# Optimization experiments

Hardware: AMD Instinct MI355X
Metric: run time of the kernel (lower is better)

## Reference

```python
import jax, jax.numpy as jnp
import numpy as np

# Fixed problem geometry: B equal-sized graphs with contiguous node ids.
B, N, E, F_IN, H, C = 64, 1024, 655360, 128, 128, 10
K1 = int(np.ceil(0.8 * N))    # 820 nodes/graph kept by pool1
K2 = int(np.ceil(0.8 * K1))   # 656 nodes/graph kept by pool2


def setup_inputs() -> dict:
    key = jax.random.key(0)
    ks = jax.random.split(key, 12)
    x = jax.random.normal(ks[0], (B * N, F_IN), jnp.float32)
    # intra-graph random edges, E//B per graph
    e_per = E // B
    local = jax.random.randint(ks[1], (2, E), 0, N)
    off = jnp.repeat(jnp.arange(B, dtype=jnp.int32) * N, e_per)
    edge_index = (local + off[None, :]).astype(jnp.int32)
    batch = jnp.repeat(jnp.arange(B, dtype=jnp.int32), N)

    def lin(k, i, o):
        return jax.random.normal(k, (i, o), jnp.float32) / np.sqrt(i)

    return {
        "x": x, "edge_index": edge_index, "batch": batch,
        "Wl1": lin(ks[2], F_IN, H), "bl1": jnp.zeros((H,), jnp.float32), "Wr1": lin(ks[3], F_IN, H),
        "Wl2": lin(ks[4], H, H),    "bl2": jnp.zeros((H,), jnp.float32), "Wr2": lin(ks[5], H, H),
        "pw1": jax.random.normal(ks[6], (H,), jnp.float32) / np.sqrt(H),
        "pw2": jax.random.normal(ks[7], (H,), jnp.float32) / np.sqrt(H),
        "fW1": lin(ks[8], 2 * H, H), "fb1": jnp.zeros((H,), jnp.float32),
        "fW2": lin(ks[9], H, C),     "fb2": jnp.zeros((C,), jnp.float32),
    }


def _sage(x, src, dst, em, Wl, bl, Wr, n):
    # PyG SAGEConv (aggr='mean'): lin_l(mean_{j->i} x_j) + lin_r(x_i)
    msg = x[src] * em[:, None]                                   # [E, d]
    s = jax.ops.segment_sum(msg, dst, num_segments=n)            # [n, d]
    cnt = jax.ops.segment_sum(em, dst, num_segments=n)           # [n]
    mean = s / jnp.maximum(cnt, 1.0)[:, None]
    return mean @ Wl + bl + x @ Wr


def _topk_pool(x, src, dst, em, n_per, k, w):
    # PyG TopKPooling: score = tanh(x.w/||w||); keep top-k per graph; gate kept x by score.
    score = jnp.tanh(x @ w / jnp.linalg.norm(w))                 # [B*n_per]
    _, idx = jax.lax.top_k(score.reshape(B, n_per), k)           # [B, k]
    idx = jnp.sort(idx, axis=1)
    perm = (idx + (jnp.arange(B) * n_per)[:, None]).reshape(-1)  # global kept ids [B*k]
    nx = x[perm] * score[perm][:, None]
    # relabel edges; drop edges touching removed nodes via mask
    inv = jnp.full((B * n_per,), -1, jnp.int32).at[perm].set(jnp.arange(B * k, dtype=jnp.int32))
    ns, nd = inv[src], inv[dst]
    nm = em * (ns >= 0).astype(x.dtype) * (nd >= 0).astype(x.dtype)
    return nx, jnp.maximum(ns, 0), jnp.maximum(nd, 0), nm


def _readout(h, k):
    g = h.reshape(B, k, H)
    return jnp.concatenate([g.mean(axis=1), g.max(axis=1)], axis=1)  # [B, 2H]


def reference(x, edge_index, batch, Wl1, bl1, Wr1, Wl2, bl2, Wr2,
              pw1, pw2, fW1, fb1, fW2, fb2):
    src, dst = edge_index[0], edge_index[1]
    em = jnp.ones((E,), x.dtype)
    h = jax.nn.relu(_sage(x, src, dst, em, Wl1, bl1, Wr1, B * N))
    h, src, dst, em = _topk_pool(h, src, dst, em, N, K1, pw1)
    x1 = _readout(h, K1)
    h = jax.nn.relu(_sage(h, src, dst, em, Wl2, bl2, Wr2, B * K1))
    h, src, dst, em = _topk_pool(h, src, dst, em, K1, K2, pw2)
    x2 = _readout(h, K2)
    z = jax.nn.relu((x1 + x2) @ fW1 + fb1)
    # dropout is identity in eval mode
    return z @ fW2 + fb2
```

## Files before the change

kernel.cpp:

```cpp
#include <hip/hip_runtime.h>
#include <cstdint>
#include <cstddef>

namespace {

constexpr int kB    = 64;
constexpr int kN    = 1024;
constexpr int kE    = 655360;
constexpr int kEper = kE / kB;
constexpr int kH    = 128;
constexpr int kK1   = 820;
constexpr int kK2   = 656;
constexpr int kM1   = kB * kN;
constexpr int kM2   = kB * kK1;
constexpr int kM3   = kB * kK2;
constexpr int kRChunks = 16;

typedef __attribute__((ext_vector_type(8))) short bf16x8;
typedef __attribute__((ext_vector_type(4))) float f32x4;

__device__ inline ushort f2bf(float f) {
  uint u = __float_as_uint(f);
  return (ushort)((u + 0x7fffu + ((u >> 16) & 1u)) >> 16);
}
__device__ inline float bf2f(ushort s) { return __uint_as_float(((uint)s) << 16); }

__device__ inline void cvt8(const float* f, uint* hh, uint* ll) {
#pragma unroll
  for (int i = 0; i < 4; ++i) {
    uint h;
    asm("v_cvt_pk_bf16_f32 %0, %1, %2" : "=v"(h) : "v"(f[2 * i]), "v"(f[2 * i + 1]));
    const float r0 = __uint_as_float(h << 16);
    const float r1 = __uint_as_float(h & 0xFFFF0000u);
    const float d0 = f[2 * i] - r0;
    const float d1 = f[2 * i + 1] - r1;
    uint l;
    asm("v_cvt_pk_bf16_f32 %0, %1, %2" : "=v"(l) : "v"(d0), "v"(d1));
    hh[i] = h; ll[i] = l;
  }
}

__device__ inline int block_scan_1024(int v, int* wsum ) {
  const int lane = threadIdx.x & 63;
  const int w    = threadIdx.x >> 6;
#pragma unroll
  for (int off = 1; off < 64; off <<= 1) {
    const int n = __shfl_up(v, off);
    if (lane >= off) v += n;
  }
  if (lane == 63) wsum[w] = v;
  __syncthreads();
  if (w == 0) {
    int s = (lane < 16) ? wsum[lane] : 0;
#pragma unroll
    for (int off = 1; off < 16; off <<= 1) {
      const int n = __shfl_up(s, off);
      if (lane >= off) s += n;
    }
    if (lane < 16) wsum[lane] = s;
  }
  __syncthreads();
  if (w > 0) v += wsum[w - 1];
  return v;
}

__global__ __launch_bounds__(1024)
void build_prep(const int* __restrict__ src, const int* __restrict__ dst,
                int* __restrict__ coff, int* __restrict__ ccur,
                int* __restrict__ ent,
                const float* __restrict__ Wl1, const float* __restrict__ Wr1,
                const float* __restrict__ Wl2, const float* __restrict__ Wr2,
                const float* __restrict__ pw1, const float* __restrict__ pw2,
                ushort* __restrict__ W1h, ushort* __restrict__ W1l,
                ushort* __restrict__ W2h, ushort* __restrict__ W2l,
                float* __restrict__ pwn1, float* __restrict__ pwn2) {
  const int b   = blockIdx.x;
  const int tid = threadIdx.x;
  if (b >= 128) {
    if (tid >= 256) return;
    const float* pw = (tid < 128) ? pw1 : pw2;
    float* o        = (tid < 128) ? pwn1 : pwn2;
    const int j = tid & 127;
    float sum = 0.0f;
    for (int k = 0; k < 128; ++k) { const float v = pw[k]; sum += v * v; }
    o[j] = pw[j] / sqrtf(sum);
    return;
  }
  if (b >= 64) {
    const int ob  = (b - 64) * 4 + (tid >> 8);
    const bool l2 = ob >= 128;
    const int idx = (ob & 127) * 256 + (tid & 255);
    const int n = idx >> 8, k = idx & 255;
    const float* Wl = l2 ? Wl2 : Wl1;
    const float* Wr = l2 ? Wr2 : Wr1;
    const float w = (k < 128) ? Wl[k * kH + n] : Wr[(k - 128) * kH + n];
    const ushort h = f2bf(w);
    (l2 ? W2h : W1h)[n * 256 + k] = h;
    (l2 ? W2l : W1l)[n * 256 + k] = f2bf(w - bf2f(h));
    return;
  }
  __shared__ int cnt[1024];
  __shared__ int wsum[16];
  const int g = b;
  const int ebase = g * kEper;
  cnt[tid] = 0;
  __syncthreads();
  for (int e = tid; e < kEper; e += 1024)
    atomicAdd(&cnt[dst[ebase + e] & (kN - 1)], 1);
  __syncthreads();
  const int dg   = cnt[tid];
  const int incl = block_scan_1024(dg, wsum);
  const int start = ebase + incl - dg;
  coff[g * kN + tid] = start;
  ccur[g * kN + tid] = start + dg;
  __syncthreads();
  cnt[tid] = start;
  __syncthreads();
  for (int e = tid; e < kEper; e += 1024) {
    const int d   = dst[ebase + e] & (kN - 1);
    const int pos = atomicAdd(&cnt[d], 1);
    ent[pos] = src[ebase + e] & (kN - 1);
  }
}

__global__ __launch_bounds__(1024, 8)
void gather1_lds(const float* __restrict__ feat, const int* __restrict__ ent,
                 const int* __restrict__ off, const int* __restrict__ cursor,
                 float* __restrict__ aggout) {
  __shared__ float cache[1024 * 16];
  const int xcd   = blockIdx.x & 7;
  const int local = blockIdx.x >> 3;
  const int graph = xcd * 8 + (local >> 3);
  const int chunk = local & 7;
  const int tid   = threadIdx.x;
  const int gbase = graph << 10;

#pragma unroll
  for (int ps = 0; ps < 4; ++ps) {
    const int row = ps * 256 + (tid >> 2);
    const int q   = (tid & 3) * 4;
    const float4 v = *(const float4*)(feat + (size_t)(gbase + row) * kH + chunk * 16 + q);
    *(float4*)&cache[row * 16 + q] = v;
  }
  __syncthreads();

  const int grp = tid >> 2;
  const int q4  = (tid & 3) * 4;

  for (int it = 0; it < 4; ++it) {
    const int lnode = it * 256 + grp;
    const int node  = gbase + lnode;
    const int o0 = off[node];
    const int o1 = cursor[node];
    const int deg = o1 - o0;
    float4 acc = make_float4(0.f, 0.f, 0.f, 0.f);
    int pf[4];
#pragma unroll
    for (int i = 0; i < 4; ++i) pf[i] = (o0 + i < o1) ? ent[o0 + i] : 0;
    for (int eb = 0; eb < deg; eb += 4) {
      int nx[4];
#pragma unroll
      for (int i = 0; i < 4; ++i) {
        const int idx = o0 + eb + 4 + i;
        nx[i] = (idx < o1) ? ent[idx] : 0;
      }
#pragma unroll
      for (int i = 0; i < 4; ++i) {
        const float m = (eb + i < deg) ? 1.0f : 0.0f;
        const float4 v = *(const float4*)&cache[pf[i] * 16 + q4];
        acc.x = fmaf(v.x, m, acc.x);
        acc.y = fmaf(v.y, m, acc.y);
        acc.z = fmaf(v.z, m, acc.z);
        acc.w = fmaf(v.w, m, acc.w);
      }
#pragma unroll
      for (int i = 0; i < 4; ++i) pf[i] = nx[i];
    }
    const float r = 1.0f / fmaxf((float)deg, 1.0f);
    const f32x4 res = {acc.x * r, acc.y * r, acc.z * r, acc.w * r};
    __builtin_nontemporal_store(res, (f32x4*)(aggout + (size_t)node * kH + chunk * 16 + q4));
  }
}

__global__ __launch_bounds__(1024, 8)
void gather2_lds(const float* __restrict__ feat, const int* __restrict__ ent,
                 const int* __restrict__ off, const int* __restrict__ cursor,
                 const int* __restrict__ perm, const float* __restrict__ gsg,
                 float* __restrict__ aggout) {
  __shared__ float cache[1024 * 16];
  __shared__ float gs[1024];
  const int xcd   = blockIdx.x & 7;
  const int local = blockIdx.x >> 3;
  const int graph = xcd * 8 + (local >> 3);
  const int chunk = local & 7;
  const int tid   = threadIdx.x;
  const int gbase = graph << 10;

#pragma unroll
  for (int ps = 0; ps < 4; ++ps) {
    const int row = ps * 256 + (tid >> 2);
    const int q   = (tid & 3) * 4;
    const float4 v = *(const float4*)(feat + (size_t)(gbase + row) * kH + chunk * 16 + q);
    *(float4*)&cache[row * 16 + q] = v;
  }
  gs[tid] = gsg[gbase + tid];
  __syncthreads();

  const int grp = tid >> 2;
  const int q4  = (tid & 3) * 4;

  for (int it = 0; it < 4; ++it) {
    const int lnode = it * 256 + grp;
    int o0 = 0, o1 = 0;
    if (lnode < kK1) {
      const int orig = perm[graph * kK1 + lnode];
      o0 = off[orig];
      o1 = cursor[orig];
    }
    const int deg = o1 - o0;
    float4 acc = make_float4(0.f, 0.f, 0.f, 0.f);
    int cnt = 0;
    int pf[4];
#pragma unroll
    for (int i = 0; i < 4; ++i) pf[i] = (o0 + i < o1) ? ent[o0 + i] : 0;
    for (int eb = 0; eb < deg; eb += 4) {
      int nx[4];
#pragma unroll
      for (int i = 0; i < 4; ++i) {
        const int idx = o0 + eb + 4 + i;
        nx[i] = (idx < o1) ? ent[idx] : 0;
      }
#pragma unroll
      for (int i = 0; i < 4; ++i) {
        const float raw  = gs[pf[i]];
        const bool  kept = (raw > 0.5f) && (eb + i < deg);
        const float s    = kept ? raw - 2.0f : 0.0f;
        cnt += kept ? 1 : 0;
        const float4 v = *(const float4*)&cache[pf[i] * 16 + q4];
        acc.x = fmaf(v.x, s, acc.x);
        acc.y = fmaf(v.y, s, acc.y);
        acc.z = fmaf(v.z, s, acc.z);
        acc.w = fmaf(v.w, s, acc.w);
      }
#pragma unroll
      for (int i = 0; i < 4; ++i) pf[i] = nx[i];
    }
    const float r = 1.0f / fmaxf((float)cnt, 1.0f);
    const f32x4 res = {acc.x * r, acc.y * r, acc.z * r, acc.w * r};
    if (lnode < kK1)
      __builtin_nontemporal_store(res,
          (f32x4*)(aggout + (size_t)(graph * kK1 + lnode) * kH + chunk * 16 + q4));
  }
}

__global__ __launch_bounds__(256)
void sage_gemm_mfma(const float* __restrict__ meanb, const float* __restrict__ xsrc,
                    const int* __restrict__ perm, const float* __restrict__ gsc,
                    const ushort* __restrict__ WTh, const ushort* __restrict__ WTl,
                    const float* __restrict__ bias, const float* __restrict__ pwn,
                    float* __restrict__ outp, float* __restrict__ scr) {
  __shared__ __align__(16) ushort aH[2][64][32];
  __shared__ __align__(16) ushort aL[2][64][32];
  __shared__ float sdot[64][2];
  const int tid  = threadIdx.x;
  const int wid  = tid >> 6;
  const int lane = tid & 63;
  const int quad = lane >> 4;
  const int l16  = lane & 15;
  const int rowbase = blockIdx.x * 64;
  const int wr = (wid >> 1) * 32;
  const int wc = (wid & 1) * 64;

  const int arow = tid >> 2;
  const int k8   = (tid & 3) * 8;
  const int grow = rowbase + arow;
  int prow = grow; float pscale = 1.0f;
  if (perm) { prow = perm[grow]; pscale = gsc[grow]; }
  const float* mrow = meanb + (size_t)grow * kH;
  const float* xrow = xsrc + (size_t)prow * kH;

  f32x4 acc[2][4];
#pragma unroll
  for (int a = 0; a < 2; ++a)
#pragma unroll
    for (int b = 0; b < 4; ++b) acc[a][b] = (f32x4){0.f, 0.f, 0.f, 0.f};

  for (int s = 0; s < 8; ++s) {
    const bool ismean = s < 4;
    const float* sp = ismean ? mrow : xrow;
    const float sc  = ismean ? 1.0f : pscale;
    const int kloc  = (ismean ? s : s - 4) * 32;
    const float4 va = *(const float4*)(sp + kloc + k8);
    const float4 vb = *(const float4*)(sp + kloc + k8 + 4);
    float f[8] = {va.x * sc, va.y * sc, va.z * sc, va.w * sc,
                  vb.x * sc, vb.y * sc, vb.z * sc, vb.w * sc};
    uint hh[4], ll[4];
    cvt8(f, hh, ll);
    *(uint4*)&aH[s & 1][arow][k8] = make_uint4(hh[0], hh[1], hh[2], hh[3]);
    *(uint4*)&aL[s & 1][arow][k8] = make_uint4(ll[0], ll[1], ll[2], ll[3]);
    __syncthreads();
    bf16x8 afh[2], afl[2];
#pragma unroll
    for (int rt = 0; rt < 2; ++rt) {
      afh[rt] = *(const bf16x8*)&aH[s & 1][wr + rt * 16 + l16][quad * 8];
      afl[rt] = *(const bf16x8*)&aL[s & 1][wr + rt * 16 + l16][quad * 8];
    }
    const int kbase = s * 32;
    bf16x8 bh[4], bl[4];
#pragma unroll
    for (int ct = 0; ct < 4; ++ct) {
      const size_t wo = (size_t)(wc + ct * 16 + l16) * 256 + kbase + quad * 8;
      bh[ct] = *(const bf16x8*)(WTh + wo);
      bl[ct] = *(const bf16x8*)(WTl + wo);
    }
#pragma unroll
    for (int ct = 0; ct < 4; ++ct) {
#pragma unroll
      for (int rt = 0; rt < 2; ++rt) {
        acc[rt][ct] = __builtin_amdgcn_mfma_f32_16x16x32_bf16(afh[rt], bh[ct], acc[rt][ct], 0, 0, 0);
        acc[rt][ct] = __builtin_amdgcn_mfma_f32_16x16x32_bf16(afh[rt], bl[ct], acc[rt][ct], 0, 0, 0);
        acc[rt][ct] = __builtin_amdgcn_mfma_f32_16x16x32_bf16(afl[rt], bh[ct], acc[rt][ct], 0, 0, 0);
      }
    }
  }
  float bv[4], pwv[4];
#pragma unroll
  for (int ct = 0; ct < 4; ++ct) {
    const int col = wc + ct * 16 + l16;
    bv[ct]  = bias[col];
    pwv[ct] = pwn[col];
  }
  float dot[2][4];
#pragma unroll
  for (int rt = 0; rt < 2; ++rt)
#pragma unroll
    for (int reg = 0; reg < 4; ++reg) dot[rt][reg] = 0.0f;
#pragma unroll
  for (int ct = 0; ct < 4; ++ct) {
    const int col = wc + ct * 16 + l16;
#pragma unroll
    for (int rt = 0; rt < 2; ++rt) {
#pragma unroll
      for (int reg = 0; reg < 4; ++reg) {
        const int row = rowbase + wr + rt * 16 + quad * 4 + reg;
        const float o = fmaxf(acc[rt][ct][reg] + bv[ct], 0.0f);
        outp[(size_t)row * kH + col] = o;
        dot[rt][reg] += o * pwv[ct];
      }
    }
  }
#pragma unroll
  for (int rt = 0; rt < 2; ++rt) {
#pragma unroll
    for (int reg = 0; reg < 4; ++reg) {
      float d = dot[rt][reg];
      d += __shfl_xor(d, 1);
      d += __shfl_xor(d, 2);
      d += __shfl_xor(d, 4);
      d += __shfl_xor(d, 8);
      if (l16 == 0) sdot[wr + rt * 16 + quad * 4 + reg][wc >> 6] = d;
    }
  }
  __syncthreads();
  if (tid < 64) scr[rowbase + tid] = tanhf(sdot[tid][0] + sdot[tid][1]);
}

__global__ __launch_bounds__(1024)
void rank_compact(const float* __restrict__ scr, int n_per, int K,
                  int* __restrict__ perm, float* __restrict__ gsc,
                  float* __restrict__ gsg) {
  __shared__ int hist[256];
  __shared__ int wsum[16];
  __shared__ uint bT;
  __shared__ int bRem;
  const int g = blockIdx.x, tid = threadIdx.x;
  const float sc = (tid < n_per) ? scr[g * n_per + tid] : -3e30f;
  const uint bits = __float_as_uint(sc);
  const uint key = (bits & 0x80000000u) ? ~bits : (bits | 0x80000000u);

  uint prefix = 0;
  int rem = K;
#pragma unroll
  for (int shift = 24; shift >= 0; shift -= 8) {
    if (tid < 256) hist[tid] = 0;
    __syncthreads();
    const uint mask = (shift == 24) ? 0u : (0xFFFFFFFFu << (shift + 8));
    if ((key & mask) == prefix)
      atomicAdd(&hist[(key >> shift) & 255], 1);
    __syncthreads();
    if (tid < 64) {
      const int h0 = hist[4 * tid + 0], h1 = hist[4 * tid + 1];
      const int h2 = hist[4 * tid + 2], h3 = hist[4 * tid + 3];
      const int loc = h0 + h1 + h2 + h3;
      int suf = loc;
#pragma unroll
      for (int d = 1; d < 64; d <<= 1) {
        const int o = __shfl_down(suf, d);
        if (tid + d < 64) suf += o;
      }
      const int above = suf - loc;
      int hs[5];
      hs[4] = above;
      hs[3] = above + h3;
      hs[2] = hs[3] + h2;
      hs[1] = hs[2] + h1;
      hs[0] = hs[1] + h0;
#pragma unroll
      for (int q = 0; q < 4; ++q) {
        if (hs[q] >= rem && hs[q + 1] < rem) {
          bT   = prefix | ((uint)(4 * tid + q) << shift);
          bRem = rem - hs[q + 1];
        }
      }
    }
    __syncthreads();
    prefix = bT;
    rem    = bRem;
  }
  const int gt = (key > prefix) ? 1 : 0;
  const int eq = (key == prefix) ? 1 : 0;
  const int incl = block_scan_1024((gt << 11) | eq, wsum);
  const int excl = incl - ((gt << 11) | eq);
  const int gt_excl = excl >> 11;
  const int eq_excl = excl & 2047;
  const int keep = (tid < n_per) && (gt || (eq && eq_excl < rem));
  if (keep) {
    const int pos = gt_excl + min(eq_excl, rem);
    perm[g * K + pos] = g * n_per + tid;
    gsc[g * K + pos]  = sc;
  }
  if (gsg) gsg[g * kN + tid] = keep ? sc + 2.0f : 0.0f;
}

__global__ __launch_bounds__(256)
void readout_part(const float* __restrict__ h, const int* __restrict__ perm,
                  const float* __restrict__ gsc, int K,
                  float* __restrict__ psum, float* __restrict__ pmax) {
  const int g     = blockIdx.x >> 4;
  const int chunk = blockIdx.x & (kRChunks - 1);
  const int j     = threadIdx.x & 127;
  const int part  = threadIdx.x >> 7;
  const int rows  = (K + kRChunks - 1) / kRChunks;
  const int r0 = chunk * rows;
  const int r1 = min(r0 + rows, K);
  float sum = 0.0f, mx = -1e30f;
  for (int r = r0 + part; r < r1; r += 2) {
    const int   row = perm[g * K + r];
    const float sc  = gsc[g * K + r];
    const float v   = h[(size_t)row * kH + j] * sc;
    sum += v;
    mx = fmaxf(mx, v);
  }
  __shared__ float ss[2][128], sm[2][128];
  ss[part][j] = sum;
  sm[part][j] = mx;
  __syncthreads();
  if (part == 0) {
    sum += ss[1][j];
    mx = fmaxf(mx, sm[1][j]);
    psum[(size_t)blockIdx.x * 128 + j] = sum;
    pmax[(size_t)blockIdx.x * 128 + j] = mx;
  }
}

__global__ __launch_bounds__(128)
void final_mlp(const float* __restrict__ ps1, const float* __restrict__ pm1,
               const float* __restrict__ ps2, const float* __restrict__ pm2,
               const float* __restrict__ fW1, const float* __restrict__ fb1,
               const float* __restrict__ fW2, const float* __restrict__ fb2,
               float* __restrict__ out) {
  __shared__ float xx[256];
  __shared__ float z[128];
  const int g = blockIdx.x, tid = threadIdx.x;
  float s1 = 0.f, m1 = -1e30f, s2 = 0.f, m2 = -1e30f;
#pragma unroll
  for (int c = 0; c < kRChunks; ++c) {
    s1 += ps1[(size_t)(g * kRChunks + c) * 128 + tid];
    m1 = fmaxf(m1, pm1[(size_t)(g * kRChunks + c) * 128 + tid]);
    s2 += ps2[(size_t)(g * kRChunks + c) * 128 + tid];
    m2 = fmaxf(m2, pm2[(size_t)(g * kRChunks + c) * 128 + tid]);
  }
  xx[tid]       = s1 / (float)kK1 + s2 / (float)kK2;
  xx[tid + 128] = m1 + m2;
  __syncthreads();
  float a = fb1[tid];
  for (int k = 0; k < 256; ++k) a += xx[k] * fW1[k * 128 + tid];
  z[tid] = fmaxf(a, 0.0f);
  __syncthreads();
  if (tid < 10) {
    float o = fb2[tid];
    for (int k = 0; k < 128; ++k) o += z[k] * fW2[k * 10 + tid];
    out[g * 10 + tid] = o;
  }
}

}

extern "C" void kernel_launch(void* const* d_in, const int* in_sizes, int n_in,
                              void* d_out, int out_size, void* d_ws, size_t ws_size,
                              hipStream_t stream) {
  const float* x   = (const float*)d_in[0];
  const int*   ei  = (const int*)d_in[1];
  const float* Wl1 = (const float*)d_in[3];
  const float* bl1 = (const float*)d_in[4];
  const float* Wr1 = (const float*)d_in[5];
  const float* Wl2 = (const float*)d_in[6];
  const float* bl2 = (const float*)d_in[7];
  const float* Wr2 = (const float*)d_in[8];
  const float* pw1 = (const float*)d_in[9];
  const float* pw2 = (const float*)d_in[10];
  const float* fW1 = (const float*)d_in[11];
  const float* fb1 = (const float*)d_in[12];
  const float* fW2 = (const float*)d_in[13];
  const float* fb2 = (const float*)d_in[14];
  const int* src = ei;
  const int* dst = ei + kE;
  (void)in_sizes; (void)n_in; (void)out_size; (void)ws_size;

  char* wsb = (char*)d_ws;
  size_t off_b = 0;
  auto alloc = [&](size_t bytes) {
    void* p = wsb + off_b;
    off_b += (bytes + 255) & ~(size_t)255;
    return p;
  };
  float* bufA = (float*)alloc((size_t)kM1 * kH * 4);
  float* bufB = (float*)alloc((size_t)kM1 * kH * 4);
  float* bufC = (float*)alloc((size_t)kM2 * kH * 4);
  int*   coff = (int*)alloc((size_t)kM1 * 4);
  int*   ccur = (int*)alloc((size_t)kM1 * 4);
  int*   ent  = (int*)alloc((size_t)kE * 4);
  float* scr  = (float*)alloc((size_t)kM1 * 4);
  float* gsg  = (float*)alloc((size_t)kM1 * 4);
  int*   perm1= (int*)alloc((size_t)kM2 * 4);
  float* gsc1 = (float*)alloc((size_t)kM2 * 4);
  int*   perm2= (int*)alloc((size_t)kM3 * 4);
  float* gsc2 = (float*)alloc((size_t)kM3 * 4);
  float* psum1= (float*)alloc((size_t)kB * kRChunks * 128 * 4);
  float* pmax1= (float*)alloc((size_t)kB * kRChunks * 128 * 4);
  float* psum2= (float*)alloc((size_t)kB * kRChunks * 128 * 4);
  float* pmax2= (float*)alloc((size_t)kB * kRChunks * 128 * 4);
  ushort* wt1h = (ushort*)alloc((size_t)128 * 256 * 2);
  ushort* wt1l = (ushort*)alloc((size_t)128 * 256 * 2);
  ushort* wt2h = (ushort*)alloc((size_t)128 * 256 * 2);
  ushort* wt2l = (ushort*)alloc((size_t)128 * 256 * 2);
  float* pwn1 = (float*)alloc(128 * 4);
  float* pwn2 = (float*)alloc(128 * 4);

  build_prep<<<129, 1024, 0, stream>>>(src, dst, coff, ccur, ent,
                                       Wl1, Wr1, Wl2, Wr2, pw1, pw2,
                                       wt1h, wt1l, wt2h, wt2l, pwn1, pwn2);

  gather1_lds<<<kB * 8, 1024, 0, stream>>>(x, ent, coff, ccur, bufA);
  sage_gemm_mfma<<<kM1 / 64, 256, 0, stream>>>(bufA, x, nullptr, nullptr,
                                               wt1h, wt1l, bl1, pwn1, bufB, scr);
  rank_compact<<<kB, 1024, 0, stream>>>(scr, kN, kK1, perm1, gsc1, gsg);
  readout_part<<<kB * kRChunks, 256, 0, stream>>>(bufB, perm1, gsc1, kK1, psum1, pmax1);

  gather2_lds<<<kB * 8, 1024, 0, stream>>>(bufB, ent, coff, ccur, perm1, gsg, bufA);
  sage_gemm_mfma<<<kM2 / 64, 256, 0, stream>>>(bufA, bufB, perm1, gsc1,
                                               wt2h, wt2l, bl2, pwn2, bufC, scr);
  rank_compact<<<kB, 1024, 0, stream>>>(scr, kK1, kK2, perm2, gsc2, nullptr);
  readout_part<<<kB * kRChunks, 256, 0, stream>>>(bufC, perm2, gsc2, kK2, psum2, pmax2);

  final_mlp<<<kB, 128, 0, stream>>>(psum1, pmax1, psum2, pmax2,
                                    fW1, fb1, fW2, fb2, (float*)d_out);
}
```

Measured before the change: 291.6 us.

## Halve GEMM row tile to 32 and stage weight slices through LDS

```diff
diff --git a/kernel.cpp b/kernel.cpp
--- a/kernel.cpp
+++ b/kernel.cpp
@@ -25,9 +25,9 @@
 }
 __device__ inline float bf2f(ushort s) { return __uint_as_float(((uint)s) << 16); }
 
-__device__ inline void cvt8(const float* f, uint* hh, uint* ll) {
-#pragma unroll
-  for (int i = 0; i < 4; ++i) {
+__device__ inline void cvt4(const float* f, uint* hh, uint* ll) {
+#pragma unroll
+  for (int i = 0; i < 2; ++i) {
     uint h;
     asm("v_cvt_pk_bf16_f32 %0, %1, %2" : "=v"(h) : "v"(f[2 * i]), "v"(f[2 * i + 1]));
     const float r0 = __uint_as_float(h << 16);
@@ -253,76 +253,80 @@
   }
 }
 
-__global__ __launch_bounds__(256)
+__global__ __launch_bounds__(256, 8)
 void sage_gemm_mfma(const float* __restrict__ meanb, const float* __restrict__ xsrc,
                     const int* __restrict__ perm, const float* __restrict__ gsc,
                     const ushort* __restrict__ WTh, const ushort* __restrict__ WTl,
                     const float* __restrict__ bias, const float* __restrict__ pwn,
                     float* __restrict__ outp, float* __restrict__ scr) {
-  __shared__ __align__(16) ushort aH[2][64][32];
-  __shared__ __align__(16) ushort aL[2][64][32];
-  __shared__ float sdot[64][2];
+  __shared__ __align__(16) ushort aH[32][32];
+  __shared__ __align__(16) ushort aL[32][32];
+  __shared__ __align__(16) ushort wHs[128][32];
+  __shared__ __align__(16) ushort wLs[128][32];
   const int tid  = threadIdx.x;
   const int wid  = tid >> 6;
   const int lane = tid & 63;
   const int quad = lane >> 4;
   const int l16  = lane & 15;
-  const int rowbase = blockIdx.x * 64;
-  const int wr = (wid >> 1) * 32;
+  const int rowbase = blockIdx.x * 32;
+  const int wr = (wid >> 1) * 16;
   const int wc = (wid & 1) * 64;
 
-  const int arow = tid >> 2;
-  const int k8   = (tid & 3) * 8;
+  const int arow = tid >> 3;
+  const int k4   = (tid & 7) * 4;
   const int grow = rowbase + arow;
   int prow = grow; float pscale = 1.0f;
   if (perm) { prow = perm[grow]; pscale = gsc[grow]; }
   const float* mrow = meanb + (size_t)grow * kH;
   const float* xrow = xsrc + (size_t)prow * kH;
 
-  f32x4 acc[2][4];
-#pragma unroll
-  for (int a = 0; a < 2; ++a)
-#pragma unroll
-    for (int b = 0; b < 4; ++b) acc[a][b] = (f32x4){0.f, 0.f, 0.f, 0.f};
+  f32x4 acc[4];
+#pragma unroll
+  for (int b = 0; b < 4; ++b) acc[b] = (f32x4){0.f, 0.f, 0.f, 0.f};
 
   for (int s = 0; s < 8; ++s) {
     const bool ismean = s < 4;
     const float* sp = ismean ? mrow : xrow;
-    const float sc  = ismean ? 1.0f : pscale;
+    const float scl = ismean ? 1.0f : pscale;
     const int kloc  = (ismean ? s : s - 4) * 32;
-    const float4 va = *(const float4*)(sp + kloc + k8);
-    const float4 vb = *(const float4*)(sp + kloc + k8 + 4);
-    float f[8] = {va.x * sc, va.y * sc, va.z * sc, va.w * sc,
-                  vb.x * sc, vb.y * sc, vb.z * sc, vb.w * sc};
-    uint hh[4], ll[4];
-    cvt8(f, hh, ll);
-    *(uint4*)&aH[s & 1][arow][k8] = make_uint4(hh[0], hh[1], hh[2], hh[3]);
-    *(uint4*)&aL[s & 1][arow][k8] = make_uint4(ll[0], ll[1], ll[2], ll[3]);
+    const int kbase = s * 32;
+    const float4 va = *(const float4*)(sp + kloc + k4);
+    float f[4] = {va.x * scl, va.y * scl, va.z * scl, va.w * scl};
+    uint hh[2], ll[2];
+    cvt4(f, hh, ll);
+    ushort4 wh[4], wl[4];
+#pragma unroll
+    for (int i = 0; i < 4; ++i) {
+      const int p  = tid + i * 256;
+      const int n  = p >> 3;
+      const int wk = (p & 7) * 4;
+      wh[i] = *(const ushort4*)(WTh + n * 256 + kbase + wk);
+      wl[i] = *(const ushort4*)(WTl + n * 256 + kbase + wk);
+    }
+    *(uint2*)&aH[arow][k4] = make_uint2(hh[0], hh[1]);
+    *(uint2*)&aL[arow][k4] = make_uint2(ll[0], ll[1]);
+#pragma unroll
+    for (int i = 0; i < 4; ++i) {
+      const int p  = tid + i * 256;
+      const int n  = p >> 3;
+      const int wk = (p & 7) * 4;
+      *(ushort4*)&wHs[n][wk] = wh[i];
+      *(ushort4*)&wLs[n][wk] = wl[i];
+    }
     __syncthreads();
-    bf16x8 afh[2], afl[2];
-#pragma unroll
-    for (int rt = 0; rt < 2; ++rt) {
-      afh[rt] = *(const bf16x8*)&aH[s & 1][wr + rt * 16 + l16][quad * 8];
-      afl[rt] = *(const bf16x8*)&aL[s & 1][wr + rt * 16 + l16][quad * 8];
-    }
-    const int kbase = s * 32;
-    bf16x8 bh[4], bl[4];
+    const bf16x8 afh = *(const bf16x8*)&aH[wr + l16][quad * 8];
+    const bf16x8 afl = *(const bf16x8*)&aL[wr + l16][quad * 8];
 #pragma unroll
     for (int ct = 0; ct < 4; ++ct) {
-      const size_t wo = (size_t)(wc + ct * 16 + l16) * 256 + kbase + quad * 8;
-      bh[ct] = *(const bf16x8*)(WTh + wo);
-      bl[ct] = *(const bf16x8*)(WTl + wo);
-    }
-#pragma unroll
-    for (int ct = 0; ct < 4; ++ct) {
-#pragma unroll
-      for (int rt = 0; rt < 2; ++rt) {
-        acc[rt][ct] = __builtin_amdgcn_mfma_f32_16x16x32_bf16(afh[rt], bh[ct], acc[rt][ct], 0, 0, 0);
-        acc[rt][ct] = __builtin_amdgcn_mfma_f32_16x16x32_bf16(afh[rt], bl[ct], acc[rt][ct], 0, 0, 0);
-        acc[rt][ct] = __builtin_amdgcn_mfma_f32_16x16x32_bf16(afl[rt], bh[ct], acc[rt][ct], 0, 0, 0);
-      }
-    }
-  }
+      const bf16x8 bh = *(const bf16x8*)&wHs[wc + ct * 16 + l16][quad * 8];
+      const bf16x8 bl = *(const bf16x8*)&wLs[wc + ct * 16 + l16][quad * 8];
+      acc[ct] = __builtin_amdgcn_mfma_f32_16x16x32_bf16(afh, bh, acc[ct], 0, 0, 0);
+      acc[ct] = __builtin_amdgcn_mfma_f32_16x16x32_bf16(afh, bl, acc[ct], 0, 0, 0);
+      acc[ct] = __builtin_amdgcn_mfma_f32_16x16x32_bf16(afl, bh, acc[ct], 0, 0, 0);
+    }
+    __syncthreads();
+  }
+  float* sdot = (float*)aH;
   float bv[4], pwv[4];
 #pragma unroll
   for (int ct = 0; ct < 4; ++ct) {
@@ -330,39 +334,29 @@
     bv[ct]  = bias[col];
     pwv[ct] = pwn[col];
   }
-  float dot[2][4];
-#pragma unroll
-  for (int rt = 0; rt < 2; ++rt)
-#pragma unroll
-    for (int reg = 0; reg < 4; ++reg) dot[rt][reg] = 0.0f;
+  float dot[4] = {0.f, 0.f, 0.f, 0.f};
 #pragma unroll
   for (int ct = 0; ct < 4; ++ct) {
     const int col = wc + ct * 16 + l16;
 #pragma unroll
-    for (int rt = 0; rt < 2; ++rt) {
-#pragma unroll
-      for (int reg = 0; reg < 4; ++reg) {
-        const int row = rowbase + wr + rt * 16 + quad * 4 + reg;
-        const float o = fmaxf(acc[rt][ct][reg] + bv[ct], 0.0f);
-        outp[(size_t)row * kH + col] = o;
-        dot[rt][reg] += o * pwv[ct];
-      }
-    }
-  }
-#pragma unroll
-  for (int rt = 0; rt < 2; ++rt) {
-#pragma unroll
     for (int reg = 0; reg < 4; ++reg) {
-      float d = dot[rt][reg];
-      d += __shfl_xor(d, 1);
-      d += __shfl_xor(d, 2);
-      d += __shfl_xor(d, 4);
-      d += __shfl_xor(d, 8);
-      if (l16 == 0) sdot[wr + rt * 16 + quad * 4 + reg][wc >> 6] = d;
-    }
-  }
-  __syncthreads();
-  if (tid < 64) scr[rowbase + tid] = tanhf(sdot[tid][0] + sdot[tid][1]);
+      const int row = rowbase + wr + quad * 4 + reg;
+      const float o = fmaxf(acc[ct][reg] + bv[ct], 0.0f);
+      outp[(size_t)row * kH + col] = o;
+      dot[reg] += o * pwv[ct];
+    }
+  }
+#pragma unroll
+  for (int reg = 0; reg < 4; ++reg) {
+    float d = dot[reg];
+    d += __shfl_xor(d, 1);
+    d += __shfl_xor(d, 2);
+    d += __shfl_xor(d, 4);
+    d += __shfl_xor(d, 8);
+    if (l16 == 0) sdot[(wr + quad * 4 + reg) * 2 + (wc >> 6)] = d;
+  }
+  __syncthreads();
+  if (tid < 32) scr[rowbase + tid] = tanhf(sdot[tid * 2] + sdot[tid * 2 + 1]);
 }
 
 __global__ __launch_bounds__(1024)
@@ -552,13 +546,13 @@
                                        wt1h, wt1l, wt2h, wt2l, pwn1, pwn2);
 
   gather1_lds<<<kB * 8, 1024, 0, stream>>>(x, ent, coff, ccur, bufA);
-  sage_gemm_mfma<<<kM1 / 64, 256, 0, stream>>>(bufA, x, nullptr, nullptr,
+  sage_gemm_mfma<<<kM1 / 32, 256, 0, stream>>>(bufA, x, nullptr, nullptr,
                                                wt1h, wt1l, bl1, pwn1, bufB, scr);
   rank_compact<<<kB, 1024, 0, stream>>>(scr, kN, kK1, perm1, gsc1, gsg);
   readout_part<<<kB * kRChunks, 256, 0, stream>>>(bufB, perm1, gsc1, kK1, psum1, pmax1);
 
   gather2_lds<<<kB * 8, 1024, 0, stream>>>(bufB, ent, coff, ccur, perm1, gsg, bufA);
-  sage_gemm_mfma<<<kM2 / 64, 256, 0, stream>>>(bufA, bufB, perm1, gsc1,
+  sage_gemm_mfma<<<kM2 / 32, 256, 0, stream>>>(bufA, bufB, perm1, gsc1,
                                                wt2h, wt2l, bl2, pwn2, bufC, scr);
   rank_compact<<<kB, 1024, 0, stream>>>(scr, kK1, kK2, perm2, gsc2, nullptr);
   readout_part<<<kB * kRChunks, 256, 0, stream>>>(bufC, perm2, gsc2, kK2, psum2, pmax2);
```

Measured after the change: 335.4 us. 15.0% more time.

## Stage full bf16 weights in LDS and load A fragments directly in SAGE GEMM

Applied to the files above, without the earlier changes.

```diff
diff --git a/kernel.cpp b/kernel.cpp
--- a/kernel.cpp
+++ b/kernel.cpp
@@ -38,6 +38,12 @@
     asm("v_cvt_pk_bf16_f32 %0, %1, %2" : "=v"(l) : "v"(d0), "v"(d1));
     hh[i] = h; ll[i] = l;
   }
+}
+
+__device__ inline bf16x8 pack8(const uint* h) {
+  union { uint u[4]; bf16x8 v; } t;
+  t.u[0] = h[0]; t.u[1] = h[1]; t.u[2] = h[2]; t.u[3] = h[3];
+  return t.v;
 }
 
 __device__ inline int block_scan_1024(int v, int* wsum ) {
@@ -253,96 +259,109 @@
   }
 }
 
-__global__ __launch_bounds__(256)
+__global__ __launch_bounds__(1024, 4)
 void sage_gemm_mfma(const float* __restrict__ meanb, const float* __restrict__ xsrc,
                     const int* __restrict__ perm, const float* __restrict__ gsc,
                     const ushort* __restrict__ WTh, const ushort* __restrict__ WTl,
                     const float* __restrict__ bias, const float* __restrict__ pwn,
                     float* __restrict__ outp, float* __restrict__ scr) {
-  __shared__ __align__(16) ushort aH[2][64][32];
-  __shared__ __align__(16) ushort aL[2][64][32];
-  __shared__ float sdot[64][2];
+  __shared__ __align__(16) ushort wfH[32768];
+  __shared__ __align__(16) ushort wfL[32768];
+  __shared__ float sdot[256][4];
   const int tid  = threadIdx.x;
+  const int lane = tid & 63;
   const int wid  = tid >> 6;
-  const int lane = tid & 63;
+  const int rg   = wid >> 2;
+  const int cg   = wid & 3;
   const int quad = lane >> 4;
   const int l16  = lane & 15;
-  const int rowbase = blockIdx.x * 64;
-  const int wr = (wid >> 1) * 32;
-  const int wc = (wid & 1) * 64;
-
-  const int arow = tid >> 2;
-  const int k8   = (tid & 3) * 8;
-  const int grow = rowbase + arow;
-  int prow = grow; float pscale = 1.0f;
-  if (perm) { prow = perm[grow]; pscale = gsc[grow]; }
-  const float* mrow = meanb + (size_t)grow * kH;
-  const float* xrow = xsrc + (size_t)prow * kH;
-
-  f32x4 acc[2][4];
-#pragma unroll
-  for (int a = 0; a < 2; ++a)
-#pragma unroll
-    for (int b = 0; b < 4; ++b) acc[a][b] = (f32x4){0.f, 0.f, 0.f, 0.f};
-
+  const int rowbase = blockIdx.x * 256;
+
+#pragma unroll
+  for (int i = 0; i < 4; ++i) {
+    const int c  = tid + i * 1024;
+    const int l  = c & 63;
+    const int s  = (c >> 6) & 7;
+    const int cf = c >> 9;
+    const int n  = cf * 16 + (l & 15);
+    const int ks = s * 32 + (l >> 4) * 8;
+    *(uint4*)&wfH[c * 8] = *(const uint4*)(WTh + n * 256 + ks);
+    *(uint4*)&wfL[c * 8] = *(const uint4*)(WTl + n * 256 + ks);
+  }
+
+  int grow[4], prow[4];
+  float pscale[4];
+#pragma unroll
+  for (int rt = 0; rt < 4; ++rt) {
+    grow[rt] = rowbase + rg * 64 + rt * 16 + l16;
+    prow[rt] = grow[rt];
+    pscale[rt] = 1.0f;
+    if (perm) { prow[rt] = perm[grow[rt]]; pscale[rt] = gsc[grow[rt]]; }
+  }
+  __syncthreads();
+
+  const ushort* wHb = wfH + cg * 8192 + lane * 8;
+  const ushort* wLb = wfL + cg * 8192 + lane * 8;
+
+  f32x4 acc[4][2];
+#pragma unroll
+  for (int rt = 0; rt < 4; ++rt)
+#pragma unroll
+    for (int ct = 0; ct < 2; ++ct) acc[rt][ct] = (f32x4){0.f, 0.f, 0.f, 0.f};
+
+#pragma unroll
   for (int s = 0; s < 8; ++s) {
     const bool ismean = s < 4;
-    const float* sp = ismean ? mrow : xrow;
-    const float sc  = ismean ? 1.0f : pscale;
-    const int kloc  = (ismean ? s : s - 4) * 32;
-    const float4 va = *(const float4*)(sp + kloc + k8);
-    const float4 vb = *(const float4*)(sp + kloc + k8 + 4);
-    float f[8] = {va.x * sc, va.y * sc, va.z * sc, va.w * sc,
-                  vb.x * sc, vb.y * sc, vb.z * sc, vb.w * sc};
-    uint hh[4], ll[4];
-    cvt8(f, hh, ll);
-    *(uint4*)&aH[s & 1][arow][k8] = make_uint4(hh[0], hh[1], hh[2], hh[3]);
-    *(uint4*)&aL[s & 1][arow][k8] = make_uint4(ll[0], ll[1], ll[2], ll[3]);
-    __syncthreads();
-    bf16x8 afh[2], afl[2];
-#pragma unroll
-    for (int rt = 0; rt < 2; ++rt) {
-      afh[rt] = *(const bf16x8*)&aH[s & 1][wr + rt * 16 + l16][quad * 8];
-      afl[rt] = *(const bf16x8*)&aL[s & 1][wr + rt * 16 + l16][quad * 8];
-    }
-    const int kbase = s * 32;
-    bf16x8 bh[4], bl[4];
-#pragma unroll
-    for (int ct = 0; ct < 4; ++ct) {
-      const size_t wo = (size_t)(wc + ct * 16 + l16) * 256 + kbase + quad * 8;
-      bh[ct] = *(const bf16x8*)(WTh + wo);
-      bl[ct] = *(const bf16x8*)(WTl + wo);
-    }
-#pragma unroll
-    for (int ct = 0; ct < 4; ++ct) {
-#pragma unroll
-      for (int rt = 0; rt < 2; ++rt) {
-        acc[rt][ct] = __builtin_amdgcn_mfma_f32_16x16x32_bf16(afh[rt], bh[ct], acc[rt][ct], 0, 0, 0);
-        acc[rt][ct] = __builtin_amdgcn_mfma_f32_16x16x32_bf16(afh[rt], bl[ct], acc[rt][ct], 0, 0, 0);
-        acc[rt][ct] = __builtin_amdgcn_mfma_f32_16x16x32_bf16(afl[rt], bh[ct], acc[rt][ct], 0, 0, 0);
-      }
-    }
-  }
-  float bv[4], pwv[4];
-#pragma unroll
-  for (int ct = 0; ct < 4; ++ct) {
-    const int col = wc + ct * 16 + l16;
+    const int kf = (ismean ? s : s - 4) * 32 + quad * 8;
+    bf16x8 ah[4], al[4];
+#pragma unroll
+    for (int rt = 0; rt < 4; ++rt) {
+      const float* rp = ismean ? (meanb + (size_t)grow[rt] * kH)
+                               : (xsrc + (size_t)prow[rt] * kH);
+      const float4 v0 = *(const float4*)(rp + kf);
+      const float4 v1 = *(const float4*)(rp + kf + 4);
+      const float scl = ismean ? 1.0f : pscale[rt];
+      float f[8] = {v0.x * scl, v0.y * scl, v0.z * scl, v0.w * scl,
+                    v1.x * scl, v1.y * scl, v1.z * scl, v1.w * scl};
+      uint hh[4], ll[4];
+      cvt8(f, hh, ll);
+      ah[rt] = pack8(hh);
+      al[rt] = pack8(ll);
+    }
+#pragma unroll
+    for (int ct = 0; ct < 2; ++ct) {
+      const bf16x8 bh = *(const bf16x8*)(wHb + (ct * 8 + s) * 512);
+      const bf16x8 bl = *(const bf16x8*)(wLb + (ct * 8 + s) * 512);
+#pragma unroll
+      for (int rt = 0; rt < 4; ++rt) {
+        acc[rt][ct] = __builtin_amdgcn_mfma_f32_16x16x32_bf16(ah[rt], bh, acc[rt][ct], 0, 0, 0);
+        acc[rt][ct] = __builtin_amdgcn_mfma_f32_16x16x32_bf16(ah[rt], bl, acc[rt][ct], 0, 0, 0);
+        acc[rt][ct] = __builtin_amdgcn_mfma_f32_16x16x32_bf16(al[rt], bh, acc[rt][ct], 0, 0, 0);
+      }
+    }
+  }
+
+  const int colbase = cg * 32;
+  float bv[2], pwv[2];
+#pragma unroll
+  for (int ct = 0; ct < 2; ++ct) {
+    const int col = colbase + ct * 16 + l16;
     bv[ct]  = bias[col];
     pwv[ct] = pwn[col];
   }
-  float dot[2][4];
-#pragma unroll
-  for (int rt = 0; rt < 2; ++rt)
+  float dot[4][4];
+#pragma unroll
+  for (int rt = 0; rt < 4; ++rt)
 #pragma unroll
     for (int reg = 0; reg < 4; ++reg) dot[rt][reg] = 0.0f;
 #pragma unroll
-  for (int ct = 0; ct < 4; ++ct) {
-    const int col = wc + ct * 16 + l16;
-#pragma unroll
-    for (int rt = 0; rt < 2; ++rt) {
+  for (int ct = 0; ct < 2; ++ct) {
+    const int col = colbase + ct * 16 + l16;
+#pragma unroll
+    for (int rt = 0; rt < 4; ++rt) {
 #pragma unroll
       for (int reg = 0; reg < 4; ++reg) {
-        const int row = rowbase + wr + rt * 16 + quad * 4 + reg;
+        const int row = rowbase + rg * 64 + rt * 16 + quad * 4 + reg;
         const float o = fmaxf(acc[rt][ct][reg] + bv[ct], 0.0f);
         outp[(size_t)row * kH + col] = o;
         dot[rt][reg] += o * pwv[ct];
@@ -350,7 +369,7 @@
     }
   }
 #pragma unroll
-  for (int rt = 0; rt < 2; ++rt) {
+  for (int rt = 0; rt < 4; ++rt) {
 #pragma unroll
     for (int reg = 0; reg < 4; ++reg) {
       float d = dot[rt][reg];
@@ -358,11 +377,14 @@
       d += __shfl_xor(d, 2);
       d += __shfl_xor(d, 4);
       d += __shfl_xor(d, 8);
-      if (l16 == 0) sdot[wr + rt * 16 + quad * 4 + reg][wc >> 6] = d;
-    }
-  }
-  __syncthreads();
-  if (tid < 64) scr[rowbase + tid] = tanhf(sdot[tid][0] + sdot[tid][1]);
+      if (l16 == 0) sdot[rg * 64 + rt * 16 + quad * 4 + reg][cg] = d;
+    }
+  }
+  __syncthreads();
+  if (tid < 256) {
+    const float4 sd = *(const float4*)&sdot[tid][0];
+    scr[rowbase + tid] = tanhf(sd.x + sd.y + sd.z + sd.w);
+  }
 }
 
 __global__ __launch_bounds__(1024)
@@ -552,14 +574,14 @@
                                        wt1h, wt1l, wt2h, wt2l, pwn1, pwn2);
 
   gather1_lds<<<kB * 8, 1024, 0, stream>>>(x, ent, coff, ccur, bufA);
-  sage_gemm_mfma<<<kM1 / 64, 256, 0, stream>>>(bufA, x, nullptr, nullptr,
-                                               wt1h, wt1l, bl1, pwn1, bufB, scr);
+  sage_gemm_mfma<<<kM1 / 256, 1024, 0, stream>>>(bufA, x, nullptr, nullptr,
+                                                 wt1h, wt1l, bl1, pwn1, bufB, scr);
   rank_compact<<<kB, 1024, 0, stream>>>(scr, kN, kK1, perm1, gsc1, gsg);
   readout_part<<<kB * kRChunks, 256, 0, stream>>>(bufB, perm1, gsc1, kK1, psum1, pmax1);
 
   gather2_lds<<<kB * 8, 1024, 0, stream>>>(bufB, ent, coff, ccur, perm1, gsg, bufA);
-  sage_gemm_mfma<<<kM2 / 64, 256, 0, stream>>>(bufA, bufB, perm1, gsc1,
-                                               wt2h, wt2l, bl2, pwn2, bufC, scr);
+  sage_gemm_mfma<<<kM2 / 256, 1024, 0, stream>>>(bufA, bufB, perm1, gsc1,
+                                                 wt2h, wt2l, bl2, pwn2, bufC, scr);
   rank_compact<<<kB, 1024, 0, stream>>>(scr, kK1, kK2, perm2, gsc2, nullptr);
   readout_part<<<kB * kRChunks, 256, 0, stream>>>(bufC, perm2, gsc2, kK2, psum2, pmax2);
 
```

Result: no change. 295.3 us (+1.3%).
